# Performance work log

Measured on AMD Instinct MI355X. Metric: run time of the kernel, lower is better.

Reference implementation:

```python
import jax, jax.numpy as jnp
import numpy as np

N_NODES = 50000
N_EDGES = 800000
N_GRAPHS = 256
NEG_SLOPE = 0.2
EPS = 1e-16


def gat_layer(x, W, a_src, a_dst, b, src, dst, num_nodes):
    # x: [N, Cin]; W: [H, Cin, Cout]; a_src/a_dst: [H, Cout]; b: [Cout]
    h = jnp.einsum('nc,hco->nho', x, W)                    # [N, H, Cout]
    e_src = jnp.einsum('nho,ho->nh', h, a_src)             # [N, H]
    e_dst = jnp.einsum('nho,ho->nh', h, a_dst)
    e = jax.nn.leaky_relu(e_src[src] + e_dst[dst], NEG_SLOPE)  # [E, H]
    # softmax over incoming edges of each destination node
    e_max = jax.ops.segment_max(e, dst, num_segments=num_nodes)
    e_max = jnp.where(jnp.isfinite(e_max), e_max, 0.0)
    w = jnp.exp(e - e_max[dst])                            # [E, H]
    denom = jax.ops.segment_sum(w, dst, num_segments=num_nodes)
    alpha = w / (denom[dst] + EPS)                         # [E, H]
    msg = h[src] * alpha[:, :, None]                       # [E, H, Cout]
    out = jax.ops.segment_sum(msg, dst, num_segments=num_nodes)  # [N, H, Cout]
    return out.mean(axis=1) + b                            # head-average (concat=False)


def setup_inputs() -> dict:
    key = jax.random.key(0)
    ks = jax.random.split(key, 16)
    H = 2
    inp = {
        'x': jax.random.normal(ks[0], (N_NODES, 16), dtype=jnp.float32),
        'edge_index': jax.random.randint(ks[1], (2, N_EDGES), 0, N_NODES, dtype=jnp.int64),
        'batch': jnp.sort(jax.random.randint(ks[2], (N_NODES,), 0, N_GRAPHS, dtype=jnp.int64)),
        'fc0_w': jax.random.normal(ks[3], (16, 32), dtype=jnp.float32) * 0.1,
        'fc0_b': jnp.zeros((32,), dtype=jnp.float32),
        'W1': jax.random.normal(ks[4], (H, 32, 64), dtype=jnp.float32) * 0.1,
        'a_src1': jax.random.normal(ks[5], (H, 64), dtype=jnp.float32) * 0.1,
        'a_dst1': jax.random.normal(ks[6], (H, 64), dtype=jnp.float32) * 0.1,
        'b1': jnp.zeros((64,), dtype=jnp.float32),
        'W2': jax.random.normal(ks[7], (H, 64, 128), dtype=jnp.float32) * 0.1,
        'a_src2': jax.random.normal(ks[8], (H, 128), dtype=jnp.float32) * 0.1,
        'a_dst2': jax.random.normal(ks[9], (H, 128), dtype=jnp.float32) * 0.1,
        'b2': jnp.zeros((128,), dtype=jnp.float32),
        'lo_w': jax.random.normal(ks[10], (128, 24), dtype=jnp.float32) * 0.1,
        'lo_b': jnp.zeros((24,), dtype=jnp.float32),
    }
    return inp


def reference(x, edge_index, batch, fc0_w, fc0_b, W1, a_src1, a_dst1, b1,
              W2, a_src2, a_dst2, b2, lo_w, lo_b):
    src, dst = edge_index[0], edge_index[1]
    h = jax.nn.elu(x @ fc0_w + fc0_b)                       # [N, 32]
    h = jax.nn.elu(gat_layer(h, W1, a_src1, a_dst1, b1, src, dst, N_NODES))  # [N, 64]
    h = jax.nn.elu(gat_layer(h, W2, a_src2, a_dst2, b2, src, dst, N_NODES))  # [N, 128]
    # global mean pool over graphs
    sums = jax.ops.segment_sum(h, batch, num_segments=N_GRAPHS)             # [G, 128]
    cnts = jax.ops.segment_sum(jnp.ones((h.shape[0], 1), h.dtype), batch, num_segments=N_GRAPHS)
    pooled = sums / jnp.maximum(cnts, 1.0)
    return pooled @ lo_w + lo_b                              # [G, 24]
```

## Files before the change

kernel.cpp:

```cpp
#include <hip/hip_runtime.h>
#include <hip/hip_fp16.h>
#include <math.h>

#define NEG_SLOPE 0.2f
#define GAT_EPS 1e-16f
#define EPB 8192

__device__ __forceinline__ float elu_f(float x) { return x > 0.f ? x : expm1f(x); }
__device__ __forceinline__ float lrelu_f(float x) { return x > 0.f ? x : NEG_SLOPE * x; }

typedef _Float16 half2v __attribute__((ext_vector_type(2)));
typedef _Float16 half8 __attribute__((ext_vector_type(8)));
typedef float f32x4 __attribute__((ext_vector_type(4)));
typedef float f32x2 __attribute__((ext_vector_type(2)));

__device__ __forceinline__ unsigned int pack_half2(float a, float b) {
    __half2 h = __floats2half2_rn(a, b);
    return __builtin_bit_cast(unsigned int, h);
}

#if __has_builtin(__builtin_amdgcn_cvt_pk_fp8_f32) && __has_builtin(__builtin_amdgcn_cvt_pk_f32_fp8)
#define HW_FP8 1
#endif

__device__ __forceinline__ unsigned int pack_fp8x4(float a, float b, float c, float d) {
#ifdef HW_FP8
    int r = 0;
    r = __builtin_amdgcn_cvt_pk_fp8_f32(a, b, r, false);
    r = __builtin_amdgcn_cvt_pk_fp8_f32(c, d, r, true);
    return (unsigned int)r;
#else
    auto enc = [](float x) -> unsigned int {
        if (x != x) return 0x7f;
        float ax = fabsf(x);
        unsigned int s = x < 0.f ? 0x80u : 0u;
        if (ax < 0.001953125f) {
            int m = (int)(ax * 512.f + 0.5f);
            if (m > 7) m = 7;
            return s | (unsigned int)m;
        }
        if (ax >= 448.f) return s | 0x7e;
        int e; float fr = frexpf(ax, &e);
        int m = (int)(fr * 16.f + 0.5f);
        if (m == 16) { m = 8; e += 1; }
        return s | ((unsigned int)(e + 6) << 3) | (unsigned int)(m - 8);
    };
    return enc(a) | (enc(b) << 8) | (enc(c) << 16) | (enc(d) << 24);
#endif
}

template <bool HI>
__device__ __forceinline__ f32x2 fp8x2_to_f32(unsigned int v) {
#ifdef HW_FP8
    return __builtin_amdgcn_cvt_pk_f32_fp8((int)v, HI);
#else
    auto dec = [](unsigned int b) -> float {
        float s = (b & 0x80) ? -1.f : 1.f;
        int e = (b >> 3) & 0xF, m = b & 7;
        if (e == 0) return s * (float)m * 0.001953125f;
        return s * (8.f + (float)m) * exp2f((float)(e - 10));
    };
    unsigned int sh = HI ? 16 : 0;
    f32x2 r;
    r[0] = dec((v >> sh) & 0xFF);
    r[1] = dec((v >> (sh + 8)) & 0xFF);
    return r;
#endif
}

__device__ __forceinline__ void acc8_pk(uint2 v, f32x2 w01,
        f32x2& c0, f32x2& c1, f32x2& c2, f32x2& c3) {
    c0 = __builtin_elementwise_fma(w01, fp8x2_to_f32<false>(v.x), c0);
    c1 = __builtin_elementwise_fma(w01, fp8x2_to_f32<true >(v.x), c1);
    c2 = __builtin_elementwise_fma(w01, fp8x2_to_f32<false>(v.y), c2);
    c3 = __builtin_elementwise_fma(w01, fp8x2_to_f32<true >(v.y), c3);
}

__device__ __forceinline__ float halfReduceSum(float v) {
    #pragma unroll
    for (int off = 16; off > 0; off >>= 1) v += __shfl_xor(v, off, 64);
    return v;
}
__device__ __forceinline__ float quarterReduceSum(float v) {
    #pragma unroll
    for (int off = 8; off > 0; off >>= 1) v += __shfl_xor(v, off, 64);
    return v;
}

__global__ __launch_bounds__(256) void init_hist(
        float* sums, float* cnts, int N, int G,
        const float* __restrict__ W1, const float* __restrict__ as1, const float* __restrict__ ad1,
        const float* __restrict__ W2, const float* __restrict__ as2, const float* __restrict__ ad2,
        float* __restrict__ wa1, float* __restrict__ wd1,
        float* __restrict__ wa2, float* __restrict__ wd2,
        __half* __restrict__ w2t,
        const int* __restrict__ dst, int* __restrict__ bhist,
        int NB, int nbl, int E, int nInit) {
    if ((int)blockIdx.x >= nInit) {
        __shared__ int lh[256];
        int bid = blockIdx.x - nInit;
        int tid = threadIdx.x;
        lh[tid] = 0;
        __syncthreads();
        int base = bid * EPB;
        int lim = E - base; if (lim > EPB) lim = EPB;
        for (int k = tid; k < lim; k += 256)
            atomicAdd(&lh[(unsigned)dst[base + k] >> 8], 1);
        __syncthreads();
        if (tid < NB) bhist[(size_t)tid * nbl + bid] = lh[tid];
        return;
    }
    int bid = blockIdx.x;
    int i = bid * 256 + threadIdx.x;
    if (i < G * 128) sums[i] = 0.f;
    if (i < G) cnts[i] = 0.f;
    if (bid == 1) {
        for (int idx = threadIdx.x; idx < 16384; idx += 256) {
            int c2 = idx >> 6, k = idx & 63;
            w2t[idx] = __float2half(W2[(c2 & 1) * 8192 + k * 128 + (c2 >> 1)]);
        }
    }
    if (bid == nInit - 1) {
        int t = threadIdx.x;
        {
            int idx = t >> 2, part = t & 3;
            int h = idx >> 5, c = idx & 31;
            const float* w = W1 + (h * 32 + c) * 64;
            float sa = 0.f, sd = 0.f;
            #pragma unroll
            for (int o = part * 16; o < part * 16 + 16; ++o) {
                sa = fmaf(w[o], as1[h * 64 + o], sa);
                sd = fmaf(w[o], ad1[h * 64 + o], sd);
            }
            sa += __shfl_xor(sa, 1, 64); sa += __shfl_xor(sa, 2, 64);
            sd += __shfl_xor(sd, 1, 64); sd += __shfl_xor(sd, 2, 64);
            if (part == 0) { wa1[idx] = sa; wd1[idx] = sd; }
        }
        {
            int idx = t >> 1, part = t & 1;
            int h = idx >> 6, c = idx & 63;
            const float* w = W2 + (h * 64 + c) * 128;
            float sa = 0.f, sd = 0.f;
            for (int o = part * 64; o < part * 64 + 64; ++o) {
                sa = fmaf(w[o], as2[h * 128 + o], sa);
                sd = fmaf(w[o], ad2[h * 128 + o], sd);
            }
            sa += __shfl_xor(sa, 1, 64);
            sd += __shfl_xor(sd, 1, 64);
            if (part == 0) { wa2[idx] = sa; wd2[idx] = sd; }
        }
    }
}

__global__ __launch_bounds__(256) void t1_scatter(
        const int* __restrict__ srcI, const int* __restrict__ dstI,
        const int* __restrict__ bhist, int* __restrict__ bstart, int* __restrict__ ofsN,
        uint2* __restrict__ ebuf, int NB, int nbl, int E,
        const float* __restrict__ x, const float* __restrict__ w0,
        const float* __restrict__ b0, const float* __restrict__ W1,
        const float* __restrict__ wa1, const float* __restrict__ wd1,
        unsigned char* __restrict__ h1, float* __restrict__ es, float* __restrict__ ed, int N) {
    if ((int)blockIdx.x < nbl) {
        __shared__ int lbase[256];
        __shared__ int wtot4[4];
        int j = blockIdx.x;
        int tid = threadIdx.x, lane = tid & 63, wid = tid >> 6;
        int rowsum = 0, pref = 0;
        if (tid < NB) {
            const int* p = bhist + (size_t)tid * nbl;
            for (int k = 0; k < nbl; ++k) {
                int v = p[k];
                rowsum += v;
                pref += (k < j) ? v : 0;
            }
        }
        int incl = rowsum;
        #pragma unroll
        for (int off = 1; off < 64; off <<= 1) {
            int t = __shfl_up(incl, off, 64);
            if (lane >= off) incl += t;
        }
        if (lane == 63) wtot4[wid] = incl;
        __syncthreads();
        int woff = 0;
        #pragma unroll
        for (int w = 0; w < 4; ++w) if (w < wid) woff += wtot4[w];
        int excl = incl - rowsum + woff;
        if (j == 0) {
            if (tid < NB) bstart[tid] = excl;
            if (tid == 0) { bstart[NB] = E; *ofsN = E; }
        }
        lbase[tid] = excl + pref;
        __syncthreads();
        int base = j * EPB;
        int lim = E - base; if (lim > EPB) lim = EPB;
        for (int k = tid; k < lim; k += 256) {
            int d = dstI[base + k];
            int s = srcI[base + k];
            int pos = atomicAdd(&lbase[(unsigned)d >> 8], 1);
            ebuf[pos] = make_uint2((unsigned)s, (unsigned)d);
        }
        return;
    }
    __shared__ float xs[8 * 16];
    __shared__ float hs[8 * 32];
    __shared__ float ws[4096];
    __shared__ float hs2[8 * 128];
    int n0 = (blockIdx.x - nbl) * 8;
    int tid = threadIdx.x;
    {
        const float4* wv4 = reinterpret_cast<const float4*>(W1);
        float4* ws4 = reinterpret_cast<float4*>(ws);
        #pragma unroll
        for (int i = 0; i < 4; ++i) ws4[tid + i * 256] = wv4[tid + i * 256];
    }
    if (tid < 128) {
        int gi = n0 * 16 + tid;
        xs[tid] = (gi < N * 16) ? x[gi] : 0.f;
    }
    __syncthreads();
    {
        int j = tid >> 5, o = tid & 31;
        float acc = b0[o];
        #pragma unroll
        for (int c = 0; c < 16; ++c) acc = fmaf(xs[j * 16 + c], w0[c * 32 + o], acc);
        hs[j * 32 + o] = elu_f(acc);
    }
    __syncthreads();
    int o = tid & 63, h = (tid >> 6) & 1, nh = tid >> 7;
    float acc[4];
    #pragma unroll
    for (int j = 0; j < 4; ++j) acc[j] = 0.f;
    const float* wp = ws + h * 2048 + o;
    #pragma unroll
    for (int c = 0; c < 32; ++c) {
        float wv = wp[c * 64];
        #pragma unroll
        for (int j = 0; j < 4; ++j) acc[j] = fmaf(hs[(nh * 4 + j) * 32 + c], wv, acc[j]);
    }
    #pragma unroll
    for (int j = 0; j < 4; ++j)
        hs2[(nh * 4 + j) * 128 + 2 * o + h] = acc[j];
    if (tid < 32) {
        int n = tid >> 2, r = tid & 3, hh = r >> 1, isd = r & 1;
        const float* wv = (isd ? wd1 : wa1) + hh * 32;
        float s = 0.f;
        #pragma unroll
        for (int c = 0; c < 32; ++c) s = fmaf(hs[n * 32 + c], wv[c], s);
        int nn = n0 + n;
        if (nn < N) { if (isd) ed[nn * 2 + hh] = s; else es[nn * 2 + hh] = s; }
    }
    __syncthreads();
    if (tid < 128) {
        int nloc = tid >> 4, cg = tid & 15;
        int n = n0 + nloc;
        if (n < N) {
            const float* p = hs2 + nloc * 128 + cg * 8;
            uint2 pk;
            pk.x = pack_fp8x4(p[0], p[1], p[2], p[3]);
            pk.y = pack_fp8x4(p[4], p[5], p[6], p[7]);
            *reinterpret_cast<uint2*>(h1 + (size_t)n * 128 + cg * 8) = pk;
        }
    }
}

__global__ __launch_bounds__(256) void bucket_csr(
        const uint2* __restrict__ ebuf, const int* __restrict__ bstart,
        const int* __restrict__ batch, float* __restrict__ cnts,
        int* __restrict__ ofs, int* __restrict__ sperm, int N) {
    __shared__ int fh[256];
    __shared__ int wtot[4];
    __shared__ int lc[256];
    int bin = blockIdx.x;
    int tid = threadIdx.x, lane = tid & 63, wid = tid >> 6;
    int ebeg = bstart[bin], eend = bstart[bin + 1];
    fh[tid] = 0;
    __syncthreads();
    for (int i = ebeg + tid; i < eend; i += 256)
        atomicAdd(&fh[ebuf[i].y & 255], 1);
    __syncthreads();
    int v = fh[tid];
    int incl = v;
    #pragma unroll
    for (int off = 1; off < 64; off <<= 1) {
        int t = __shfl_up(incl, off, 64);
        if (lane >= off) incl += t;
    }
    if (lane == 63) wtot[wid] = incl;
    __syncthreads();
    int woff = 0;
    #pragma unroll
    for (int w = 0; w < 4; ++w) if (w < wid) woff += wtot[w];
    int excl = incl - v + woff;
    int d = (bin << 8) + tid;
    if (d < N) ofs[d] = ebeg + excl;
    lc[tid] = excl;
    if (d < N) {
        int b = batch[d];
        int b0 = __shfl(b, 0, 64);
        if (__all(b == b0)) {
            unsigned long long m = __ballot(1);
            if (lane == 0) atomicAdd(&cnts[b], (float)__popcll(m));
        } else {
            atomicAdd(&cnts[b], 1.f);
        }
    }
    __syncthreads();
    for (int i = ebeg + tid; i < eend; i += 256) {
        uint2 e = ebuf[i];
        int pos = atomicAdd(&lc[e.y & 255], 1);
        sperm[ebeg + pos] = (int)e.x;
    }
}

__global__ __launch_bounds__(256) void t2_mfma(
        const __half* __restrict__ g1h,
        const __half* __restrict__ w2t,
        unsigned char* __restrict__ h8, int N) {
    __shared__ __half sbuf[16384];
    int tid = threadIdx.x;
    {
        const uint4* srcv = reinterpret_cast<const uint4*>(w2t);
        #pragma unroll
        for (int i = 0; i < 8; ++i) {
            int idx = tid + i * 256;
            int row = idx >> 3;
            int byteoff = (idx * 16) ^ ((row & 7) << 4);
            *reinterpret_cast<uint4*>(reinterpret_cast<char*>(sbuf) + byteoff) = srcv[idx];
        }
    }
    __syncthreads();
    int w = tid >> 6, lane = tid & 63;
    int r = lane & 15, kg = lane >> 4;
    int nodei = blockIdx.x * 64 + w * 16 + r;
    const half8* ap = reinterpret_cast<const half8*>(
        reinterpret_cast<const _Float16*>(g1h) + (size_t)nodei * 64 + kg * 8);

    f32x4 acc[16];
    #pragma unroll
    for (int nf = 0; nf < 16; ++nf) acc[nf] = f32x4{0.f, 0.f, 0.f, 0.f};
    half8 az = {};
    #pragma unroll
    for (int ks = 0; ks < 2; ++ks) {
        half8 a = (nodei < N) ? ap[ks * 4] : az;
        #pragma unroll
        for (int nf = 0; nf < 16; ++nf) {
            int brow = nf * 16 + r;
            int bbyte = (brow * 128 + ks * 64 + kg * 16) ^ ((brow & 7) << 4);
            half8 b = *reinterpret_cast<const half8*>(reinterpret_cast<const char*>(sbuf) + bbyte);
            acc[nf] = __builtin_amdgcn_mfma_f32_16x16x32_f16(a, b, acc[nf], 0, 0, 0);
        }
    }
    #pragma unroll
    for (int q = 0; q < 4; ++q) {
        int n = blockIdx.x * 64 + w * 16 + kg * 4 + q;
        if (n < N) {
            uint4 pk;
            pk.x = pack_fp8x4(acc[0][q],  acc[1][q],  acc[2][q],  acc[3][q]);
            pk.y = pack_fp8x4(acc[4][q],  acc[5][q],  acc[6][q],  acc[7][q]);
            pk.z = pack_fp8x4(acc[8][q],  acc[9][q],  acc[10][q], acc[11][q]);
            pk.w = pack_fp8x4(acc[12][q], acc[13][q], acc[14][q], acc[15][q]);
            *reinterpret_cast<uint4*>(h8 + (size_t)n * 256 + r * 16) = pk;
        }
    }
}

__global__ __launch_bounds__(256) void gat_agg1(
        const int* __restrict__ ofs, const int* __restrict__ sperm,
        const float* __restrict__ es, const float* __restrict__ ed,
        const uint2* __restrict__ h1v, const float* __restrict__ b1,
        const float* __restrict__ wa2, const float* __restrict__ wd2,
        uint2* __restrict__ g1h, float* __restrict__ es2, float* __restrict__ ed2, int N) {
    __shared__ uint2 meta[16][32];
    int q = threadIdx.x >> 4;
    int d = blockIdx.x * 16 + q;
    int lane = threadIdx.x & 15;
    bool active = d < N;
    if (!active) return;
    float2 edv = *reinterpret_cast<const float2*>(ed + (size_t)d * 2);
    int beg = ofs[d], end = ofs[d + 1];
    int deg = end - beg;
    int jmax = deg < 32 ? deg : 32;

    int s0i = 0, s1i = 0;
    float ex00 = 0.f, ex01 = 0.f, ex10 = 0.f, ex11 = 0.f;
    int i0 = beg + lane, i1 = beg + lane + 16;
    if (i0 < end) {
        s0i = sperm[i0];
        float2 e = *reinterpret_cast<const float2*>(es + (size_t)s0i * 2);
        ex00 = __expf(lrelu_f(e.x + edv.x));
        ex01 = __expf(lrelu_f(e.y + edv.y));
    }
    if (i1 < end) {
        s1i = sperm[i1];
        float2 e = *reinterpret_cast<const float2*>(es + (size_t)s1i * 2);
        ex10 = __expf(lrelu_f(e.x + edv.x));
        ex11 = __expf(lrelu_f(e.y + edv.y));
    }
    float s0 = ex00 + ex10, s1 = ex01 + ex11;
    for (int i = i0 + 32; i < end; i += 16) {
        int s = sperm[i];
        float2 e = *reinterpret_cast<const float2*>(es + (size_t)s * 2);
        s0 += __expf(lrelu_f(e.x + edv.x));
        s1 += __expf(lrelu_f(e.y + edv.y));
    }
    s0 = quarterReduceSum(s0);
    s1 = quarterReduceSum(s1);
    float r0 = 0.5f / (s0 + GAT_EPS), r1 = 0.5f / (s1 + GAT_EPS);
    if (lane < jmax)
        meta[q][lane] = make_uint2((unsigned int)s0i, pack_half2(ex00 * r0, ex01 * r1));
    if (lane + 16 < jmax)
        meta[q][lane + 16] = make_uint2((unsigned int)s1i, pack_half2(ex10 * r0, ex11 * r1));

    f32x2 c0{0.f, 0.f}, c1{0.f, 0.f}, c2{0.f, 0.f}, c3{0.f, 0.f};
    int j = 0;
    for (; j + 8 <= jmax; j += 8) {
        uint2 vv[8];
        #pragma unroll
        for (int k = 0; k < 8; ++k) vv[k] = h1v[(size_t)meta[q][j + k].x * 16 + lane];
        #pragma unroll
        for (int k = 0; k < 8; ++k) {
            float2 af = __half22float2(__builtin_bit_cast(__half2, meta[q][j + k].y));
            acc8_pk(vv[k], f32x2{af.x, af.y}, c0, c1, c2, c3);
        }
    }
    for (; j + 4 <= jmax; j += 4) {
        uint2 vv[4];
        #pragma unroll
        for (int k = 0; k < 4; ++k) vv[k] = h1v[(size_t)meta[q][j + k].x * 16 + lane];
        #pragma unroll
        for (int k = 0; k < 4; ++k) {
            float2 af = __half22float2(__builtin_bit_cast(__half2, meta[q][j + k].y));
            acc8_pk(vv[k], f32x2{af.x, af.y}, c0, c1, c2, c3);
        }
    }
    for (; j < jmax; ++j) {
        uint2 m = meta[q][j];
        float2 af = __half22float2(__builtin_bit_cast(__half2, m.y));
        acc8_pk(h1v[(size_t)m.x * 16 + lane], f32x2{af.x, af.y}, c0, c1, c2, c3);
    }
    for (int i = beg + 32; i < end; ++i) {
        int s = sperm[i];
        float2 e = *reinterpret_cast<const float2*>(es + (size_t)s * 2);
        float w0 = __expf(lrelu_f(e.x + edv.x)) * r0;
        float w1 = __expf(lrelu_f(e.y + edv.y)) * r1;
        acc8_pk(h1v[(size_t)s * 16 + lane], f32x2{w0, w1}, c0, c1, c2, c3);
    }
    float a0 = c0[0] + c0[1], a1 = c1[0] + c1[1];
    float a2 = c2[0] + c2[1], a3 = c3[0] + c3[1];
    float4 bv = reinterpret_cast<const float4*>(b1)[lane];
    float o0 = elu_f(a0 + bv.x);
    float o1 = elu_f(a1 + bv.y);
    float o2 = elu_f(a2 + bv.z);
    float o3 = elu_f(a3 + bv.w);
    g1h[(size_t)d * 16 + lane] = make_uint2(pack_half2(o0, o1), pack_half2(o2, o3));
    float4 wa0 = reinterpret_cast<const float4*>(wa2)[lane];
    float4 wa1v = reinterpret_cast<const float4*>(wa2)[16 + lane];
    float4 wd0 = reinterpret_cast<const float4*>(wd2)[lane];
    float4 wd1v = reinterpret_cast<const float4*>(wd2)[16 + lane];
    float p0 = o0 * wa0.x + o1 * wa0.y + o2 * wa0.z + o3 * wa0.w;
    float p1 = o0 * wa1v.x + o1 * wa1v.y + o2 * wa1v.z + o3 * wa1v.w;
    float q0 = o0 * wd0.x + o1 * wd0.y + o2 * wd0.z + o3 * wd0.w;
    float q1 = o0 * wd1v.x + o1 * wd1v.y + o2 * wd1v.z + o3 * wd1v.w;
    p0 = quarterReduceSum(p0);
    p1 = quarterReduceSum(p1);
    q0 = quarterReduceSum(q0);
    q1 = quarterReduceSum(q1);
    if (lane == 0) {
        es2[(size_t)d * 2]     = p0;
        es2[(size_t)d * 2 + 1] = p1;
        ed2[(size_t)d * 2]     = q0;
        ed2[(size_t)d * 2 + 1] = q1;
    }
}

__global__ __launch_bounds__(256) void gat_agg2(
        const int* __restrict__ ofs, const int* __restrict__ sperm,
        const float* __restrict__ es, const float* __restrict__ ed,
        const uint2* __restrict__ h8v, const float* __restrict__ b2,
        const int* __restrict__ batch, float* __restrict__ sums, int N) {
    __shared__ uint2 meta[8][32];
    __shared__ float louts[8 * 128];
    __shared__ int lbat[8];
    int half = threadIdx.x >> 5;
    int d = blockIdx.x * 8 + half;
    int lane = threadIdx.x & 31;
    bool active = d < N;
    int beg = 0, end = 0;
    if (active) {
        beg = ofs[d]; end = ofs[d + 1];
        if (lane == 0) lbat[half] = batch[d];
    } else if (lane == 0) {
        lbat[half] = -1;
    }
    float2 edv = active ? *reinterpret_cast<const float2*>(ed + (size_t)d * 2)
                        : make_float2(0.f, 0.f);
    int deg = end - beg;
    int jmax = deg < 32 ? deg : 32;

    int s_f = 0;
    float ex0 = 0.f, ex1 = 0.f;
    int i0 = beg + lane;
    if (i0 < end) {
        s_f = sperm[i0];
        float2 esv = *reinterpret_cast<const float2*>(es + (size_t)s_f * 2);
        ex0 = __expf(lrelu_f(esv.x + edv.x));
        ex1 = __expf(lrelu_f(esv.y + edv.y));
    }
    float s0 = ex0, s1 = ex1;
    for (int i = i0 + 32; i < end; i += 32) {
        int s = sperm[i];
        float2 esv = *reinterpret_cast<const float2*>(es + (size_t)s * 2);
        s0 += __expf(lrelu_f(esv.x + edv.x));
        s1 += __expf(lrelu_f(esv.y + edv.y));
    }
    s0 = halfReduceSum(s0);
    s1 = halfReduceSum(s1);
    float r0 = 0.5f / (s0 + GAT_EPS), r1 = 0.5f / (s1 + GAT_EPS);
    if (lane < jmax)
        meta[half][lane] = make_uint2((unsigned int)s_f, pack_half2(ex0 * r0, ex1 * r1));

    int head = (lane >> 1) & 1;
    f32x2 c0{0.f, 0.f}, c1{0.f, 0.f}, c2{0.f, 0.f}, c3{0.f, 0.f};

    int j = 0;
    for (; j + 8 <= jmax; j += 8) {
        uint2 vv[8];
        #pragma unroll
        for (int k = 0; k < 8; ++k) vv[k] = h8v[(size_t)meta[half][j + k].x * 32 + lane];
        #pragma unroll
        for (int k = 0; k < 8; ++k) {
            float2 af = __half22float2(__builtin_bit_cast(__half2, meta[half][j + k].y));
            float av = head ? af.y : af.x;
            acc8_pk(vv[k], f32x2{av, av}, c0, c1, c2, c3);
        }
    }
    for (; j < jmax; ++j) {
        uint2 v = h8v[(size_t)meta[half][j].x * 32 + lane];
        float2 af = __half22float2(__builtin_bit_cast(__half2, meta[half][j].y));
        float av = head ? af.y : af.x;
        acc8_pk(v, f32x2{av, av}, c0, c1, c2, c3);
    }
    for (int i = beg + 32; i < end; ++i) {
        int s = sperm[i];
        float2 esv = *reinterpret_cast<const float2*>(es + (size_t)s * 2);
        float a0 = __expf(lrelu_f(esv.x + edv.x)) * r0;
        float a1 = __expf(lrelu_f(esv.y + edv.y)) * r1;
        float av = head ? a1 : a0;
        acc8_pk(h8v[(size_t)s * 32 + lane], f32x2{av, av}, c0, c1, c2, c3);
    }
    float acc[8] = { c0[0], c0[1], c1[0], c1[1], c2[0], c2[1], c3[0], c3[1] };
    #pragma unroll
    for (int i = 0; i < 8; ++i) acc[i] += __shfl_xor(acc[i], 2, 64);
    if (head == 0) {
        int jch = lane >> 2;
        int nfb = (lane & 1) * 8;
        #pragma unroll
        for (int i = 0; i < 8; ++i) {
            int o = (nfb + i) * 8 + jch;
            louts[half * 128 + o] = active ? elu_f(acc[i] + b2[o]) : 0.f;
        }
    }
    __syncthreads();
    if (threadIdx.x < 128) {
        int c = threadIdx.x;
        int cur = lbat[0];
        float a = 0.f;
        #pragma unroll
        for (int n = 0; n < 8; ++n) {
            int b = lbat[n];
            if (b != cur) {
                if (cur >= 0) atomicAdd(&sums[(size_t)cur * 128 + c], a);
                a = 0.f; cur = b;
            }
            a += louts[n * 128 + c];
        }
        if (cur >= 0) atomicAdd(&sums[(size_t)cur * 128 + c], a);
    }
}

__global__ void final_kernel(
        const float* __restrict__ sums, const float* __restrict__ cnts,
        const float* __restrict__ w, const float* __restrict__ b,
        float* __restrict__ out, int G) {
    int g = blockIdx.x;
    int k = threadIdx.x;
    if (k >= 24) return;
    float inv = 1.f / fmaxf(cnts[g], 1.f);
    float acc = b[k];
    #pragma unroll
    for (int c = 0; c < 128; ++c) acc = fmaf(sums[g * 128 + c] * inv, w[c * 24 + k], acc);
    out[g * 24 + k] = acc;
}

extern "C" void kernel_launch(void* const* d_in, const int* in_sizes, int n_in,
                              void* d_out, int out_size, void* d_ws, size_t ws_size,
                              hipStream_t stream) {
    const float* x      = (const float*)d_in[0];
    const int*   ei     = (const int*)d_in[1];
    const int*   batch  = (const int*)d_in[2];
    const float* fc0_w  = (const float*)d_in[3];
    const float* fc0_b  = (const float*)d_in[4];
    const float* W1     = (const float*)d_in[5];
    const float* a_src1 = (const float*)d_in[6];
    const float* a_dst1 = (const float*)d_in[7];
    const float* b1     = (const float*)d_in[8];
    const float* W2     = (const float*)d_in[9];
    const float* a_src2 = (const float*)d_in[10];
    const float* a_dst2 = (const float*)d_in[11];
    const float* b2     = (const float*)d_in[12];
    const float* lo_w   = (const float*)d_in[13];
    const float* lo_b   = (const float*)d_in[14];
    float* out = (float*)d_out;

    const int N = in_sizes[0] / 16;
    const int E = in_sizes[1] / 2;
    const int G = out_size / 24;
    const int* src = ei;
    const int* dst = ei + E;
    const int NB  = (N + 255) >> 8;
    const int nbl = (E + EPB - 1) / EPB;
    const int nInit = (N + 255) / 256;
    const int nT1 = (N + 7) / 8;

    char* wsb = (char*)d_ws;
    size_t off = 0;
    auto allocf = [&](size_t n) { float* p = (float*)(wsb + off); off += ((n * 4 + 255) & ~(size_t)255); return p; };
    auto alloci = [&](size_t n) { int* p = (int*)(wsb + off); off += ((n * 4 + 255) & ~(size_t)255); return p; };
    auto alloch = [&](size_t n) { __half* p = (__half*)(wsb + off); off += ((n * 2 + 255) & ~(size_t)255); return p; };
    __half* hbuf  = alloch((size_t)N * 256);
    __half* g1h   = alloch((size_t)(N + 64) * 64);
    __half* w2t   = alloch(16384);
    float*  es    = allocf((size_t)N * 2);
    float*  ed    = allocf((size_t)N * 2);
    float*  es2   = allocf((size_t)N * 2);
    float*  ed2   = allocf((size_t)N * 2);
    float*  sums  = allocf((size_t)G * 128);
    float*  cnts  = allocf((size_t)G);
    float*  wa1   = allocf(64);
    float*  wd1   = allocf(64);
    float*  wa2   = allocf(128);
    float*  wd2   = allocf(128);
    int* ofs     = alloci((size_t)N + 1);
    int* sperm   = alloci((size_t)E);
    int* bhist   = alloci((size_t)NB * nbl);
    int* bstart  = alloci((size_t)NB + 1);
    uint2* ebuf  = (uint2*)alloci((size_t)E * 2);
    (void)ws_size;

    init_hist<<<nInit + nbl, 256, 0, stream>>>(sums, cnts, N, G,
            W1, a_src1, a_dst1, W2, a_src2, a_dst2, wa1, wd1, wa2, wd2, w2t,
            dst, bhist, NB, nbl, E, nInit);
    t1_scatter<<<nbl + nT1, 256, 0, stream>>>(
            src, dst, bhist, bstart, ofs + N, ebuf, NB, nbl, E,
            x, fc0_w, fc0_b, W1, wa1, wd1, (unsigned char*)hbuf, es, ed, N);
    bucket_csr<<<NB, 256, 0, stream>>>(ebuf, bstart, batch, cnts, ofs, sperm, N);

    gat_agg1<<<(N + 15) / 16, 256, 0, stream>>>(ofs, sperm, es, ed, (const uint2*)hbuf, b1,
            wa2, wd2, (uint2*)g1h, es2, ed2, N);
    t2_mfma<<<(N + 63) / 64, 256, 0, stream>>>(g1h, w2t, (unsigned char*)hbuf, N);
    gat_agg2<<<(N + 7) / 8, 256, 0, stream>>>(ofs, sperm, es2, ed2, (const uint2*)hbuf, b2,
            batch, sums, N);
    final_kernel<<<G, 32, 0, stream>>>(sums, cnts, lo_w, lo_b, out, G);
}
```

Baseline: 240.9 us.

## Fuse layer-2 MFMA transform into layer-1 aggregation and pack edge buffer

Merges the separate t2_mfma kernel into the layer-1 aggregation kernel. Each 16-node block now stages its aggregated fp16 features in LDS and runs the 16x256 MFMA transform directly, so the g1h round trip through global memory and one launch go away. The edge scatter buffer is packed into one 32-bit word (src<<8 | dst&255) instead of a uint2, halving that traffic. Attention weights in shared memory are stored as float2 instead of packed half2. In exchange, W2 fragments are read from global or cache by every block rather than from swizzled LDS, and the packing assumes src fits in 24 bits.

```diff
diff --git a/kernel.cpp b/kernel.cpp
--- a/kernel.cpp
+++ b/kernel.cpp
@@ -155,7 +155,7 @@
 __global__ __launch_bounds__(256) void t1_scatter(
         const int* __restrict__ srcI, const int* __restrict__ dstI,
         const int* __restrict__ bhist, int* __restrict__ bstart, int* __restrict__ ofsN,
-        uint2* __restrict__ ebuf, int NB, int nbl, int E,
+        unsigned int* __restrict__ ebuf, int NB, int nbl, int E,
         const float* __restrict__ x, const float* __restrict__ w0,
         const float* __restrict__ b0, const float* __restrict__ W1,
         const float* __restrict__ wa1, const float* __restrict__ wd1,
@@ -198,7 +198,7 @@
             int d = dstI[base + k];
             int s = srcI[base + k];
             int pos = atomicAdd(&lbase[(unsigned)d >> 8], 1);
-            ebuf[pos] = make_uint2((unsigned)s, (unsigned)d);
+            ebuf[pos] = ((unsigned)s << 8) | ((unsigned)d & 255u);
         }
         return;
     }
@@ -265,7 +265,7 @@
 }
 
 __global__ __launch_bounds__(256) void bucket_csr(
-        const uint2* __restrict__ ebuf, const int* __restrict__ bstart,
+        const unsigned int* __restrict__ ebuf, const int* __restrict__ bstart,
         const int* __restrict__ batch, float* __restrict__ cnts,
         int* __restrict__ ofs, int* __restrict__ sperm, int N) {
     __shared__ int fh[256];
@@ -277,7 +277,7 @@
     fh[tid] = 0;
     __syncthreads();
     for (int i = ebeg + tid; i < eend; i += 256)
-        atomicAdd(&fh[ebuf[i].y & 255], 1);
+        atomicAdd(&fh[ebuf[i] & 255u], 1);
     __syncthreads();
     int v = fh[tid];
     int incl = v;
@@ -307,170 +307,157 @@
     }
     __syncthreads();
     for (int i = ebeg + tid; i < eend; i += 256) {
-        uint2 e = ebuf[i];
-        int pos = atomicAdd(&lc[e.y & 255], 1);
-        sperm[ebeg + pos] = (int)e.x;
-    }
-}
-
-__global__ __launch_bounds__(256) void t2_mfma(
-        const __half* __restrict__ g1h,
-        const __half* __restrict__ w2t,
-        unsigned char* __restrict__ h8, int N) {
-    __shared__ __half sbuf[16384];
-    int tid = threadIdx.x;
-    {
-        const uint4* srcv = reinterpret_cast<const uint4*>(w2t);
-        #pragma unroll
-        for (int i = 0; i < 8; ++i) {
-            int idx = tid + i * 256;
-            int row = idx >> 3;
-            int byteoff = (idx * 16) ^ ((row & 7) << 4);
-            *reinterpret_cast<uint4*>(reinterpret_cast<char*>(sbuf) + byteoff) = srcv[idx];
-        }
-    }
-    __syncthreads();
-    int w = tid >> 6, lane = tid & 63;
-    int r = lane & 15, kg = lane >> 4;
-    int nodei = blockIdx.x * 64 + w * 16 + r;
-    const half8* ap = reinterpret_cast<const half8*>(
-        reinterpret_cast<const _Float16*>(g1h) + (size_t)nodei * 64 + kg * 8);
-
-    f32x4 acc[16];
-    #pragma unroll
-    for (int nf = 0; nf < 16; ++nf) acc[nf] = f32x4{0.f, 0.f, 0.f, 0.f};
-    half8 az = {};
-    #pragma unroll
-    for (int ks = 0; ks < 2; ++ks) {
-        half8 a = (nodei < N) ? ap[ks * 4] : az;
-        #pragma unroll
-        for (int nf = 0; nf < 16; ++nf) {
-            int brow = nf * 16 + r;
-            int bbyte = (brow * 128 + ks * 64 + kg * 16) ^ ((brow & 7) << 4);
-            half8 b = *reinterpret_cast<const half8*>(reinterpret_cast<const char*>(sbuf) + bbyte);
-            acc[nf] = __builtin_amdgcn_mfma_f32_16x16x32_f16(a, b, acc[nf], 0, 0, 0);
-        }
-    }
-    #pragma unroll
-    for (int q = 0; q < 4; ++q) {
-        int n = blockIdx.x * 64 + w * 16 + kg * 4 + q;
-        if (n < N) {
-            uint4 pk;
-            pk.x = pack_fp8x4(acc[0][q],  acc[1][q],  acc[2][q],  acc[3][q]);
-            pk.y = pack_fp8x4(acc[4][q],  acc[5][q],  acc[6][q],  acc[7][q]);
-            pk.z = pack_fp8x4(acc[8][q],  acc[9][q],  acc[10][q], acc[11][q]);
-            pk.w = pack_fp8x4(acc[12][q], acc[13][q], acc[14][q], acc[15][q]);
-            *reinterpret_cast<uint4*>(h8 + (size_t)n * 256 + r * 16) = pk;
-        }
-    }
-}
-
-__global__ __launch_bounds__(256) void gat_agg1(
+        unsigned int e = ebuf[i];
+        int pos = atomicAdd(&lc[e & 255u], 1);
+        sperm[ebeg + pos] = (int)(e >> 8);
+    }
+}
+
+__global__ __launch_bounds__(256) void agg1_t2(
         const int* __restrict__ ofs, const int* __restrict__ sperm,
         const float* __restrict__ es, const float* __restrict__ ed,
         const uint2* __restrict__ h1v, const float* __restrict__ b1,
         const float* __restrict__ wa2, const float* __restrict__ wd2,
-        uint2* __restrict__ g1h, float* __restrict__ es2, float* __restrict__ ed2, int N) {
-    __shared__ uint2 meta[16][32];
+        const __half* __restrict__ w2t,
+        unsigned char* __restrict__ h8, float* __restrict__ es2, float* __restrict__ ed2, int N) {
+    __shared__ unsigned int meta_s[16][32];
+    __shared__ float2 meta_a[16][32];
+    __shared__ __half a_lds[16 * 64];
     int q = threadIdx.x >> 4;
-    int d = blockIdx.x * 16 + q;
+    int n0 = blockIdx.x * 16;
+    int d = n0 + q;
     int lane = threadIdx.x & 15;
     bool active = d < N;
-    if (!active) return;
-    float2 edv = *reinterpret_cast<const float2*>(ed + (size_t)d * 2);
-    int beg = ofs[d], end = ofs[d + 1];
-    int deg = end - beg;
-    int jmax = deg < 32 ? deg : 32;
-
-    int s0i = 0, s1i = 0;
-    float ex00 = 0.f, ex01 = 0.f, ex10 = 0.f, ex11 = 0.f;
-    int i0 = beg + lane, i1 = beg + lane + 16;
-    if (i0 < end) {
-        s0i = sperm[i0];
-        float2 e = *reinterpret_cast<const float2*>(es + (size_t)s0i * 2);
-        ex00 = __expf(lrelu_f(e.x + edv.x));
-        ex01 = __expf(lrelu_f(e.y + edv.y));
-    }
-    if (i1 < end) {
-        s1i = sperm[i1];
-        float2 e = *reinterpret_cast<const float2*>(es + (size_t)s1i * 2);
-        ex10 = __expf(lrelu_f(e.x + edv.x));
-        ex11 = __expf(lrelu_f(e.y + edv.y));
-    }
-    float s0 = ex00 + ex10, s1 = ex01 + ex11;
-    for (int i = i0 + 32; i < end; i += 16) {
-        int s = sperm[i];
-        float2 e = *reinterpret_cast<const float2*>(es + (size_t)s * 2);
-        s0 += __expf(lrelu_f(e.x + edv.x));
-        s1 += __expf(lrelu_f(e.y + edv.y));
-    }
-    s0 = quarterReduceSum(s0);
-    s1 = quarterReduceSum(s1);
-    float r0 = 0.5f / (s0 + GAT_EPS), r1 = 0.5f / (s1 + GAT_EPS);
-    if (lane < jmax)
-        meta[q][lane] = make_uint2((unsigned int)s0i, pack_half2(ex00 * r0, ex01 * r1));
-    if (lane + 16 < jmax)
-        meta[q][lane + 16] = make_uint2((unsigned int)s1i, pack_half2(ex10 * r0, ex11 * r1));
-
-    f32x2 c0{0.f, 0.f}, c1{0.f, 0.f}, c2{0.f, 0.f}, c3{0.f, 0.f};
-    int j = 0;
-    for (; j + 8 <= jmax; j += 8) {
-        uint2 vv[8];
-        #pragma unroll
-        for (int k = 0; k < 8; ++k) vv[k] = h1v[(size_t)meta[q][j + k].x * 16 + lane];
-        #pragma unroll
-        for (int k = 0; k < 8; ++k) {
-            float2 af = __half22float2(__builtin_bit_cast(__half2, meta[q][j + k].y));
-            acc8_pk(vv[k], f32x2{af.x, af.y}, c0, c1, c2, c3);
-        }
-    }
-    for (; j + 4 <= jmax; j += 4) {
-        uint2 vv[4];
-        #pragma unroll
-        for (int k = 0; k < 4; ++k) vv[k] = h1v[(size_t)meta[q][j + k].x * 16 + lane];
-        #pragma unroll
-        for (int k = 0; k < 4; ++k) {
-            float2 af = __half22float2(__builtin_bit_cast(__half2, meta[q][j + k].y));
-            acc8_pk(vv[k], f32x2{af.x, af.y}, c0, c1, c2, c3);
-        }
-    }
-    for (; j < jmax; ++j) {
-        uint2 m = meta[q][j];
-        float2 af = __half22float2(__builtin_bit_cast(__half2, m.y));
-        acc8_pk(h1v[(size_t)m.x * 16 + lane], f32x2{af.x, af.y}, c0, c1, c2, c3);
-    }
-    for (int i = beg + 32; i < end; ++i) {
-        int s = sperm[i];
-        float2 e = *reinterpret_cast<const float2*>(es + (size_t)s * 2);
-        float w0 = __expf(lrelu_f(e.x + edv.x)) * r0;
-        float w1 = __expf(lrelu_f(e.y + edv.y)) * r1;
-        acc8_pk(h1v[(size_t)s * 16 + lane], f32x2{w0, w1}, c0, c1, c2, c3);
-    }
-    float a0 = c0[0] + c0[1], a1 = c1[0] + c1[1];
-    float a2 = c2[0] + c2[1], a3 = c3[0] + c3[1];
-    float4 bv = reinterpret_cast<const float4*>(b1)[lane];
-    float o0 = elu_f(a0 + bv.x);
-    float o1 = elu_f(a1 + bv.y);
-    float o2 = elu_f(a2 + bv.z);
-    float o3 = elu_f(a3 + bv.w);
-    g1h[(size_t)d * 16 + lane] = make_uint2(pack_half2(o0, o1), pack_half2(o2, o3));
-    float4 wa0 = reinterpret_cast<const float4*>(wa2)[lane];
-    float4 wa1v = reinterpret_cast<const float4*>(wa2)[16 + lane];
-    float4 wd0 = reinterpret_cast<const float4*>(wd2)[lane];
-    float4 wd1v = reinterpret_cast<const float4*>(wd2)[16 + lane];
-    float p0 = o0 * wa0.x + o1 * wa0.y + o2 * wa0.z + o3 * wa0.w;
-    float p1 = o0 * wa1v.x + o1 * wa1v.y + o2 * wa1v.z + o3 * wa1v.w;
-    float q0 = o0 * wd0.x + o1 * wd0.y + o2 * wd0.z + o3 * wd0.w;
-    float q1 = o0 * wd1v.x + o1 * wd1v.y + o2 * wd1v.z + o3 * wd1v.w;
-    p0 = quarterReduceSum(p0);
-    p1 = quarterReduceSum(p1);
-    q0 = quarterReduceSum(q0);
-    q1 = quarterReduceSum(q1);
-    if (lane == 0) {
-        es2[(size_t)d * 2]     = p0;
-        es2[(size_t)d * 2 + 1] = p1;
-        ed2[(size_t)d * 2]     = q0;
-        ed2[(size_t)d * 2 + 1] = q1;
+    float o0 = 0.f, o1 = 0.f, o2 = 0.f, o3 = 0.f;
+    if (active) {
+        float2 edv = *reinterpret_cast<const float2*>(ed + (size_t)d * 2);
+        int beg = ofs[d], end = ofs[d + 1];
+        int deg = end - beg;
+        int jmax = deg < 32 ? deg : 32;
+
+        int s0i = 0, s1i = 0;
+        float ex00 = 0.f, ex01 = 0.f, ex10 = 0.f, ex11 = 0.f;
+        int i0 = beg + lane, i1 = beg + lane + 16;
+        if (i0 < end) {
+            s0i = sperm[i0];
+            float2 e = *reinterpret_cast<const float2*>(es + (size_t)s0i * 2);
+            ex00 = __expf(lrelu_f(e.x + edv.x));
+            ex01 = __expf(lrelu_f(e.y + edv.y));
+        }
+        if (i1 < end) {
+            s1i = sperm[i1];
+            float2 e = *reinterpret_cast<const float2*>(es + (size_t)s1i * 2);
+            ex10 = __expf(lrelu_f(e.x + edv.x));
+            ex11 = __expf(lrelu_f(e.y + edv.y));
+        }
+        float s0 = ex00 + ex10, s1 = ex01 + ex11;
+        for (int i = i0 + 32; i < end; i += 16) {
+            int s = sperm[i];
+            float2 e = *reinterpret_cast<const float2*>(es + (size_t)s * 2);
+            s0 += __expf(lrelu_f(e.x + edv.x));
+            s1 += __expf(lrelu_f(e.y + edv.y));
+        }
+        s0 = quarterReduceSum(s0);
+        s1 = quarterReduceSum(s1);
+        float r0 = 0.5f / (s0 + GAT_EPS), r1 = 0.5f / (s1 + GAT_EPS);
+        if (lane < jmax) {
+            meta_s[q][lane] = (unsigned int)s0i;
+            meta_a[q][lane] = make_float2(ex00 * r0, ex01 * r1);
+        }
+        if (lane + 16 < jmax) {
+            meta_s[q][lane + 16] = (unsigned int)s1i;
+            meta_a[q][lane + 16] = make_float2(ex10 * r0, ex11 * r1);
+        }
+
+        f32x2 c0{0.f, 0.f}, c1{0.f, 0.f}, c2{0.f, 0.f}, c3{0.f, 0.f};
+        int j = 0;
+        for (; j + 8 <= jmax; j += 8) {
+            uint2 vv[8];
+            #pragma unroll
+            for (int k = 0; k < 8; ++k) vv[k] = h1v[(size_t)meta_s[q][j + k] * 16 + lane];
+            #pragma unroll
+            for (int k = 0; k < 8; ++k) {
+                float2 af = meta_a[q][j + k];
+                acc8_pk(vv[k], f32x2{af.x, af.y}, c0, c1, c2, c3);
+            }
+        }
+        for (; j + 4 <= jmax; j += 4) {
+            uint2 vv[4];
+            #pragma unroll
+            for (int k = 0; k < 4; ++k) vv[k] = h1v[(size_t)meta_s[q][j + k] * 16 + lane];
+            #pragma unroll
+            for (int k = 0; k < 4; ++k) {
+                float2 af = meta_a[q][j + k];
+                acc8_pk(vv[k], f32x2{af.x, af.y}, c0, c1, c2, c3);
+            }
+        }
+        for (; j < jmax; ++j) {
+            float2 af = meta_a[q][j];
+            acc8_pk(h1v[(size_t)meta_s[q][j] * 16 + lane], f32x2{af.x, af.y}, c0, c1, c2, c3);
+        }
+        for (int i = beg + 32; i < end; ++i) {
+            int s = sperm[i];
+            float2 e = *reinterpret_cast<const float2*>(es + (size_t)s * 2);
+            float w0 = __expf(lrelu_f(e.x + edv.x)) * r0;
+            float w1 = __expf(lrelu_f(e.y + edv.y)) * r1;
+            acc8_pk(h1v[(size_t)s * 16 + lane], f32x2{w0, w1}, c0, c1, c2, c3);
+        }
+        float a0 = c0[0] + c0[1], a1 = c1[0] + c1[1];
+        float a2 = c2[0] + c2[1], a3 = c3[0] + c3[1];
+        float4 bv = reinterpret_cast<const float4*>(b1)[lane];
+        o0 = elu_f(a0 + bv.x);
+        o1 = elu_f(a1 + bv.y);
+        o2 = elu_f(a2 + bv.z);
+        o3 = elu_f(a3 + bv.w);
+        float4 wa0 = reinterpret_cast<const float4*>(wa2)[lane];
+        float4 wa1v = reinterpret_cast<const float4*>(wa2)[16 + lane];
+        float4 wd0 = reinterpret_cast<const float4*>(wd2)[lane];
+        float4 wd1v = reinterpret_cast<const float4*>(wd2)[16 + lane];
+        float p0 = o0 * wa0.x + o1 * wa0.y + o2 * wa0.z + o3 * wa0.w;
+        float p1 = o0 * wa1v.x + o1 * wa1v.y + o2 * wa1v.z + o3 * wa1v.w;
+        float q0 = o0 * wd0.x + o1 * wd0.y + o2 * wd0.z + o3 * wd0.w;
+        float q1 = o0 * wd1v.x + o1 * wd1v.y + o2 * wd1v.z + o3 * wd1v.w;
+        p0 = quarterReduceSum(p0);
+        p1 = quarterReduceSum(p1);
+        q0 = quarterReduceSum(q0);
+        q1 = quarterReduceSum(q1);
+        if (lane == 0) {
+            es2[(size_t)d * 2]     = p0;
+            es2[(size_t)d * 2 + 1] = p1;
+            ed2[(size_t)d * 2]     = q0;
+            ed2[(size_t)d * 2 + 1] = q1;
+        }
+    }
+    {
+        int abyte = (q * 128 + lane * 8) ^ ((q & 7) << 4);
+        *reinterpret_cast<unsigned int*>(reinterpret_cast<char*>(a_lds) + abyte) = pack_half2(o0, o1);
+        *reinterpret_cast<unsigned int*>(reinterpret_cast<char*>(a_lds) + abyte + 4) = pack_half2(o2, o3);
+    }
+    __syncthreads();
+    int w = threadIdx.x >> 6, gl = threadIdx.x & 63;
+    int r = gl & 15, kg = gl >> 4;
+    f32x4 acc[4];
+    #pragma unroll
+    for (int i = 0; i < 4; ++i) acc[i] = f32x4{0.f, 0.f, 0.f, 0.f};
+    #pragma unroll
+    for (int ks = 0; ks < 2; ++ks) {
+        int abyte = (r * 128 + ks * 64 + kg * 16) ^ ((r & 7) << 4);
+        half8 a = *reinterpret_cast<const half8*>(reinterpret_cast<const char*>(a_lds) + abyte);
+        #pragma unroll
+        for (int i = 0; i < 4; ++i) {
+            int col = (w * 4 + i) * 16 + r;
+            half8 b = *reinterpret_cast<const half8*>(
+                reinterpret_cast<const _Float16*>(w2t) + col * 64 + ks * 32 + kg * 8);
+            acc[i] = __builtin_amdgcn_mfma_f32_16x16x32_f16(a, b, acc[i], 0, 0, 0);
+        }
+    }
+    #pragma unroll
+    for (int qq = 0; qq < 4; ++qq) {
+        int n = n0 + kg * 4 + qq;
+        if (n < N) {
+            unsigned int pk = pack_fp8x4(acc[0][qq], acc[1][qq], acc[2][qq], acc[3][qq]);
+            *reinterpret_cast<unsigned int*>(h8 + (size_t)n * 256 + r * 16 + w * 4) = pk;
+        }
     }
 }
 
@@ -479,7 +466,8 @@
         const float* __restrict__ es, const float* __restrict__ ed,
         const uint2* __restrict__ h8v, const float* __restrict__ b2,
         const int* __restrict__ batch, float* __restrict__ sums, int N) {
-    __shared__ uint2 meta[8][32];
+    __shared__ unsigned int meta_s[8][32];
+    __shared__ float2 meta_a[8][32];
     __shared__ float louts[8 * 128];
     __shared__ int lbat[8];
     int half = threadIdx.x >> 5;
@@ -517,8 +505,10 @@
     s0 = halfReduceSum(s0);
     s1 = halfReduceSum(s1);
     float r0 = 0.5f / (s0 + GAT_EPS), r1 = 0.5f / (s1 + GAT_EPS);
-    if (lane < jmax)
-        meta[half][lane] = make_uint2((unsigned int)s_f, pack_half2(ex0 * r0, ex1 * r1));
+    if (lane < jmax) {
+        meta_s[half][lane] = (unsigned int)s_f;
+        meta_a[half][lane] = make_float2(ex0 * r0, ex1 * r1);
+    }
 
     int head = (lane >> 1) & 1;
     f32x2 c0{0.f, 0.f}, c1{0.f, 0.f}, c2{0.f, 0.f}, c3{0.f, 0.f};
@@ -527,17 +517,17 @@
     for (; j + 8 <= jmax; j += 8) {
         uint2 vv[8];
         #pragma unroll
-        for (int k = 0; k < 8; ++k) vv[k] = h8v[(size_t)meta[half][j + k].x * 32 + lane];
+        for (int k = 0; k < 8; ++k) vv[k] = h8v[(size_t)meta_s[half][j + k] * 32 + lane];
         #pragma unroll
         for (int k = 0; k < 8; ++k) {
-            float2 af = __half22float2(__builtin_bit_cast(__half2, meta[half][j + k].y));
+            float2 af = meta_a[half][j + k];
             float av = head ? af.y : af.x;
             acc8_pk(vv[k], f32x2{av, av}, c0, c1, c2, c3);
         }
     }
     for (; j < jmax; ++j) {
-        uint2 v = h8v[(size_t)meta[half][j].x * 32 + lane];
-        float2 af = __half22float2(__builtin_bit_cast(__half2, meta[half][j].y));
+        uint2 v = h8v[(size_t)meta_s[half][j] * 32 + lane];
+        float2 af = meta_a[half][j];
         float av = head ? af.y : af.x;
         acc8_pk(v, f32x2{av, av}, c0, c1, c2, c3);
     }
@@ -628,8 +618,8 @@
     auto allocf = [&](size_t n) { float* p = (float*)(wsb + off); off += ((n * 4 + 255) & ~(size_t)255); return p; };
     auto alloci = [&](size_t n) { int* p = (int*)(wsb + off); off += ((n * 4 + 255) & ~(size_t)255); return p; };
     auto alloch = [&](size_t n) { __half* p = (__half*)(wsb + off); off += ((n * 2 + 255) & ~(size_t)255); return p; };
-    __half* hbuf  = alloch((size_t)N * 256);
-    __half* g1h   = alloch((size_t)(N + 64) * 64);
+    __half* hbuf  = alloch((size_t)N * 64);
+    __half* h8buf = alloch((size_t)N * 128);
     __half* w2t   = alloch(16384);
     float*  es    = allocf((size_t)N * 2);
     float*  ed    = allocf((size_t)N * 2);
@@ -645,7 +635,7 @@
     int* sperm   = alloci((size_t)E);
     int* bhist   = alloci((size_t)NB * nbl);
     int* bstart  = alloci((size_t)NB + 1);
-    uint2* ebuf  = (uint2*)alloci((size_t)E * 2);
+    unsigned int* ebuf = (unsigned int*)alloci((size_t)E);
     (void)ws_size;
 
     init_hist<<<nInit + nbl, 256, 0, stream>>>(sums, cnts, N, G,
@@ -656,10 +646,9 @@
             x, fc0_w, fc0_b, W1, wa1, wd1, (unsigned char*)hbuf, es, ed, N);
     bucket_csr<<<NB, 256, 0, stream>>>(ebuf, bstart, batch, cnts, ofs, sperm, N);
 
-    gat_agg1<<<(N + 15) / 16, 256, 0, stream>>>(ofs, sperm, es, ed, (const uint2*)hbuf, b1,
-            wa2, wd2, (uint2*)g1h, es2, ed2, N);
-    t2_mfma<<<(N + 63) / 64, 256, 0, stream>>>(g1h, w2t, (unsigned char*)hbuf, N);
-    gat_agg2<<<(N + 7) / 8, 256, 0, stream>>>(ofs, sperm, es2, ed2, (const uint2*)hbuf, b2,
+    agg1_t2<<<(N + 15) / 16, 256, 0, stream>>>(ofs, sperm, es, ed, (const uint2*)hbuf, b1,
+            wa2, wd2, w2t, (unsigned char*)h8buf, es2, ed2, N);
+    gat_agg2<<<(N + 7) / 8, 256, 0, stream>>>(ofs, sperm, es2, ed2, (const uint2*)h8buf, b2,
             batch, sums, N);
     final_kernel<<<G, 32, 0, stream>>>(sums, cnts, lo_w, lo_b, out, G);
 }
```

After: 256.5 us. 1.06x slower.
